# Optimization experiments

Measured on AMD Instinct MI355X. Metric: run time of the kernel, lower is better.

## Reference

```python
import jax, jax.numpy as jnp
import numpy as np

B, F, M, N, H, O = 8, 128, 256, 1024, 64, 128
BN_EPS = 1e-5
COS_EPS = 1e-8


def _bn(x, g, b, m, v):
    # inference-mode BatchNorm over channel axis 1
    shape = [1] * x.ndim
    shape[1] = -1
    return g.reshape(shape) * (x - m.reshape(shape)) * jax.lax.rsqrt(v.reshape(shape) + BN_EPS) + b.reshape(shape)


def setup_inputs() -> dict:
    key = jax.random.key(0)
    ks = jax.random.split(key, 24)
    def n(k, shape, s=1.0):
        return jax.random.normal(k, shape, dtype=jnp.float32) * s
    inp = {}
    inp['template_feature'] = n(ks[0], (B, F, M))
    inp['search_feature'] = n(ks[1], (B, F, N))
    # SharedMLP 1x1 conv weights (bias=False because bn=True)
    inp['W1'] = n(ks[2], (H, F + 1), 0.05)
    inp['W2'] = n(ks[3], (H, H), 0.05)
    inp['W3'] = n(ks[4], (H, H), 0.05)
    # fea_layer: conv1d(H, bn=True) then conv1d(O, activation=None, bias=True)
    inp['Wc1'] = n(ks[5], (H, H), 0.05)
    inp['Wc2'] = n(ks[6], (O, H), 0.05)
    inp['bc2'] = n(ks[7], (O,), 0.05)
    for i, nm in enumerate(['1', '2', '3', 'c1']):
        inp['g' + nm] = 1.0 + n(ks[8 + i], (H,), 0.1)
        inp['b' + nm] = n(ks[12 + i], (H,), 0.1)
        inp['m' + nm] = n(ks[16 + i], (H,), 0.01)
        inp['v' + nm] = jax.random.uniform(ks[20 + i], (H,), minval=0.5, maxval=1.5, dtype=jnp.float32)
    return inp


def reference(template_feature, search_feature, W1, W2, W3, Wc1, Wc2, bc2,
              g1, b1, m1, v1, g2, b2, m2, v2, g3, b3, m3, v3, gc1, bc1, mc1, vc1):
    t, s = template_feature, search_feature
    # pairwise cosine similarity over channel dim (no BxFxMxN expand needed)
    dot = jnp.einsum('bfm,bfn->bmn', t, s)
    nt = jnp.linalg.norm(t, axis=1)  # (B, M)
    ns = jnp.linalg.norm(s, axis=1)  # (B, N)
    cos = dot / jnp.maximum(nt[:, :, None] * ns[:, None, :], COS_EPS)  # (B, M, N)
    # first 1x1 conv on concat(cos, expand(t)) computed fused (no concat materialization)
    h = jnp.einsum('hf,bfm->bhm', W1[:, 1:], t)[..., None] + W1[:, 0][None, :, None, None] * cos[:, None]
    h = jax.nn.relu(_bn(h, g1, b1, m1, v1))  # (B, H, M, N)
    h = jax.nn.relu(_bn(jnp.einsum('gh,bhmn->bgmn', W2, h), g2, b2, m2, v2))
    h = jax.nn.relu(_bn(jnp.einsum('gh,bhmn->bgmn', W3, h), g3, b3, m3, v3))
    p = jnp.max(h, axis=2)  # max-pool over M -> (B, H, N)
    c = jax.nn.relu(_bn(jnp.einsum('gh,bhn->bgn', Wc1, p), gc1, bc1, mc1, vc1))
    return jnp.einsum('oh,bhn->bon', Wc2, c) + bc2[None, :, None]  # (B, O, N)
```

## Files before the change

### kernel.cpp

```cpp
#include <hip/hip_runtime.h>


#define BB 8
#define FF 128
#define MM 256
#define NN 1024
#define HH 64
#define OO 128
#define BN_EPS 1e-5f
#define COS_EPS 1e-8f

#define WS_U     0
#define WS_C2    64
#define WS_C3    128
#define WS_CC1   192
#define WS_W2H   256
#define WS_W3H   2304
#define WS_WC1F  8448
#define WS_A1    12544
#define WS_NT    143616
#define WS_NS    145664
#define WS_COSH  153856
#define WS_P     1202432
#define PS       524288

typedef _Float16 half2v __attribute__((ext_vector_type(2)));
typedef _Float16 half8  __attribute__((ext_vector_type(8)));
typedef __attribute__((ext_vector_type(4))) float f32x4;

__device__ __forceinline__ unsigned int pkh2(float a, float b){
  auto h = __builtin_amdgcn_cvt_pkrtz(a, b);
  return __builtin_bit_cast(unsigned int, h);
}
__device__ __forceinline__ half2v u2h(unsigned int u){
  return __builtin_bit_cast(half2v, u);
}
__device__ __forceinline__ unsigned int h2u(half2v v){
  return __builtin_bit_cast(unsigned int, v);
}
__device__ __forceinline__ unsigned int relu2(unsigned int d){
  half2v v = __builtin_elementwise_max(u2h(d), (half2v){(_Float16)0, (_Float16)0});
  return h2u(v);
}
__device__ __forceinline__ unsigned int bh1(unsigned int up, half2v c, unsigned int ap){
  half2v v = __builtin_elementwise_fma(u2h(up), c, u2h(ap));
  v = __builtin_elementwise_max(v, (half2v){(_Float16)0, (_Float16)0});
  return h2u(v);
}
__device__ __forceinline__ float dot4(float4 a, float4 b, float acc){
  acc = fmaf(a.x, b.x, acc); acc = fmaf(a.y, b.y, acc);
  acc = fmaf(a.z, b.z, acc); acc = fmaf(a.w, b.w, acc);
  return acc;
}

__global__ __launch_bounds__(256) void k_prep(const float* t_, const float* s_,
    const float* W1, const float* W2, const float* W3, const float* Wc1,
    const float* g1, const float* b1, const float* m1, const float* v1,
    const float* g2, const float* b2, const float* m2, const float* v2,
    const float* g3, const float* b3, const float* m3, const float* v3,
    const float* gc1,const float* bc1,const float* mc1,const float* vc1,
    float* ws){
  __shared__ float W1s[64][133];
  int t = threadIdx.x;
  int bx = blockIdx.x;
  if (bx < 256){
    int b = bx >> 5, m0 = (bx & 31)*8;
    for (int idx = t; idx < 8192; idx += 256){
      int h = idx >> 7, f = idx & 127;
      W1s[h][f] = W1[h*129 + 1 + f];
    }
    __syncthreads();
    int h = t & 63, mg = t >> 6;
    const float* tp = t_ + (size_t)b*FF*MM + m0 + mg*2;
    float acc0 = 0.f, acc1 = 0.f;
    for (int f = 0; f < FF; f++){
      float wv = W1s[h][f];
      float2 tv = *(const float2*)&tp[(size_t)f*MM];
      acc0 = fmaf(wv, tv.x, acc0); acc1 = fmaf(wv, tv.y, acc1);
    }
    float a1 = g1[h] / sqrtf(v1[h] + BN_EPS);
    float c1 = b1[h] - a1*m1[h];
    unsigned short* dst = (unsigned short*)(ws + WS_A1) + ((size_t)(b*MM + m0 + mg*2))*64 + h;
    dst[0]  = (unsigned short)(pkh2(fmaf(a1, acc0, c1), 0.f) & 0xFFFFu);
    dst[64] = (unsigned short)(pkh2(fmaf(a1, acc1, c1), 0.f) & 0xFFFFu);
  } else if (bx < 416){
    __shared__ float red[4][64];
    int x = t & 63, fq = t >> 6;
    int idx = (bx - 256)*64 + x;
    const float* ptr; size_t stride;
    if (idx < BB*MM){
      int b = idx >> 8, m = idx & 255;
      ptr = t_ + (size_t)b*FF*MM + m; stride = MM;
    } else {
      int j = idx - BB*MM;
      int b = j >> 10, n = j & 1023;
      ptr = s_ + (size_t)b*FF*NN + n; stride = NN;
    }
    float acc = 0.f;
    for (int f = fq*32; f < fq*32 + 32; f++){
      float v = ptr[(size_t)f*stride]; acc = fmaf(v, v, acc);
    }
    red[fq][x] = acc;
    __syncthreads();
    if (fq == 0)
      ws[WS_NT + idx] = sqrtf(red[0][x] + red[1][x] + red[2][x] + red[3][x]);
  } else {
    if (t < 64){
      float a1 = g1[t] / sqrtf(v1[t] + BN_EPS);
      ws[WS_U + t]   = a1 * W1[t*129];
      float a2 = g2[t] / sqrtf(v2[t] + BN_EPS);
      ws[WS_C2 + t]  = b2[t] - a2*m2[t];
      float a3 = g3[t] / sqrtf(v3[t] + BN_EPS);
      ws[WS_C3 + t]  = b3[t] - a3*m3[t];
      float ac = gc1[t] / sqrtf(vc1[t] + BN_EPS);
      ws[WS_CC1 + t] = bc1[t] - ac*mc1[t];
    }
    unsigned short* w2h = (unsigned short*)(ws + WS_W2H);
    unsigned short* w3h = (unsigned short*)(ws + WS_W3H);
    for (int i = t; i < 4096; i += 256){
      int g = i >> 6;
      float a2 = g2[g] / sqrtf(v2[g] + BN_EPS);
      w2h[i] = __builtin_bit_cast(unsigned short, (_Float16)(a2 * W2[i]));
      float a3 = g3[g] / sqrtf(v3[g] + BN_EPS);
      w3h[i] = __builtin_bit_cast(unsigned short, (_Float16)(a3 * W3[i]));
      float ac = gc1[g] / sqrtf(vc1[g] + BN_EPS);
      ws[WS_WC1F + i] = ac * Wc1[i];
    }
  }
}

__global__ __launch_bounds__(256) void k_cos(const float* t_, const float* s_, float* ws){
  __shared__ __align__(16) unsigned short tS[64][136];
  __shared__ __align__(16) unsigned short sS[64][136];
  __shared__ float ntS[64], nsS[64];
  int t = threadIdx.x;
  int lane = t & 63, w = t >> 6;
  int ln15 = lane & 15, quad = lane >> 4;
  int m0 = blockIdx.x*64, n0 = blockIdx.y*64, b = blockIdx.z;
  {
    int x = t & 63;
    const float* tb = t_ + (size_t)b*FF*MM + m0 + x;
    const float* sb = s_ + (size_t)b*FF*NN + n0 + x;
    #pragma unroll
    for (int k = 0; k < 16; k++){
      int fp = w*16 + k;
      *(unsigned int*)&tS[x][2*fp] = pkh2(tb[(size_t)(2*fp)*MM], tb[(size_t)(2*fp+1)*MM]);
      *(unsigned int*)&sS[x][2*fp] = pkh2(sb[(size_t)(2*fp)*NN], sb[(size_t)(2*fp+1)*NN]);
    }
    if (t < 64) ntS[t] = ws[WS_NT + b*MM + m0 + t];
    else if (t < 128) nsS[t-64] = ws[WS_NS + b*NN + n0 + (t-64)];
  }
  __syncthreads();
  half8 A4[4];
  #pragma unroll
  for (int kc = 0; kc < 4; kc++)
    A4[kc] = *(const half8*)&sS[w*16 + ln15][kc*32 + quad*8];
  float4 ns4 = *(const float4*)&nsS[w*16 + quad*4];
  int nb = n0 + w*16 + quad*4;
  unsigned short* cosw = (unsigned short*)(ws + WS_COSH);
  #pragma unroll
  for (int mt = 0; mt < 4; mt++){
    f32x4 acc = (f32x4){0.f,0.f,0.f,0.f};
    #pragma unroll
    for (int kc = 0; kc < 4; kc++){
      half8 B4 = *(const half8*)&tS[mt*16 + ln15][kc*32 + quad*8];
      acc = __builtin_amdgcn_mfma_f32_16x16x32_f16(A4[kc], B4, acc, 0, 0, 0);
    }
    int m = m0 + mt*16 + ln15;
    float ntv = ntS[mt*16 + ln15];
    float c0 = acc[0] * __builtin_amdgcn_rcpf(fmaxf(ntv*ns4.x, COS_EPS));
    float c1 = acc[1] * __builtin_amdgcn_rcpf(fmaxf(ntv*ns4.y, COS_EPS));
    float c2 = acc[2] * __builtin_amdgcn_rcpf(fmaxf(ntv*ns4.z, COS_EPS));
    float c3 = acc[3] * __builtin_amdgcn_rcpf(fmaxf(ntv*ns4.w, COS_EPS));
    uint2 vv;
    vv.x = pkh2(c0, c1);
    vv.y = pkh2(c2, c3);
    *(uint2*)&cosw[(size_t)(b*MM + m)*NN + nb] = vv;
  }
}

__global__ __launch_bounds__(256, 3) void k_main(const float* ws, float* Pp){
  __shared__ __align__(16) unsigned char h2B[4][2][2304];
  __shared__ __align__(16) float redS[3][16][68];
  int t = threadIdx.x;
  int lane = t & 63, w = t >> 6;
  int ln15 = lane & 15, quad = lane >> 4;
  int b = blockIdx.y;
  int n0 = blockIdx.x * 16;
  int ms = blockIdx.z;

  const unsigned short* w2h = (const unsigned short*)(ws + WS_W2H);
  const unsigned short* w3h = (const unsigned short*)(ws + WS_W3H);
  half8 W2A[4][2], W3A[4][2];
  f32x4 c2v[4];
  #pragma unroll
  for (int rt = 0; rt < 4; rt++){
    int g = rt*16 + ln15;
    #pragma unroll
    for (int kk = 0; kk < 2; kk++){
      W2A[rt][kk] = *(const half8*)&w2h[g*64 + kk*32 + quad*8];
      W3A[rt][kk] = *(const half8*)&w3h[g*64 + kk*32 + quad*8];
    }
    float4 cb2 = *(const float4*)&ws[WS_C2 + rt*16 + quad*4];
    c2v[rt] = (f32x4){cb2.x, cb2.y, cb2.z, cb2.w};
  }
  f32x4 zf = (f32x4){0.f, 0.f, 0.f, 0.f};
  unsigned int upk[2][4];
  #pragma unroll
  for (int kk = 0; kk < 2; kk++){
    float4 ua = *(const float4*)&ws[WS_U + kk*32 + quad*8];
    float4 ub = *(const float4*)&ws[WS_U + kk*32 + quad*8 + 4];
    upk[kk][0] = pkh2(ua.x, ua.y); upk[kk][1] = pkh2(ua.z, ua.w);
    upk[kk][2] = pkh2(ub.x, ub.y); upk[kk][3] = pkh2(ub.z, ub.w);
  }
  const unsigned short* A1H = (const unsigned short*)(ws + WS_A1) + (size_t)b*MM*64;
  int n = n0 + ln15;
  const unsigned short* cosP = (const unsigned short*)(ws + WS_COSH)
                               + (size_t)b*MM*NN + n;
  unsigned char* myb = &h2B[w][0][0];
  int wOff = ln15*144 + quad*8;
  int rOff = ln15*144 + quad*16;

  f32x4 p[4];
  #pragma unroll
  for (int rt = 0; rt < 4; rt++)
    p[rt] = (f32x4){-3.0e38f, -3.0e38f, -3.0e38f, -3.0e38f};

  int m0i = ms*128 + w;
  unsigned int cu = cosP[(size_t)m0i*NN];
  uint4 a1a = *(const uint4*)&A1H[(size_t)m0i*64 + quad*8];
  uint4 a1b = *(const uint4*)&A1H[(size_t)m0i*64 + 32 + quad*8];

  {
    int mN = ms*128 + 4 + w;
    unsigned int cuN = cosP[(size_t)mN*NN];
    uint4 a1aN = *(const uint4*)&A1H[(size_t)mN*64 + quad*8];
    uint4 a1bN = *(const uint4*)&A1H[(size_t)mN*64 + 32 + quad*8];
    unsigned int cd = cu | (cu << 16);
    half2v ch = u2h(cd);
    uint4 q0, q1;
    q0.x = bh1(upk[0][0], ch, a1a.x); q0.y = bh1(upk[0][1], ch, a1a.y);
    q0.z = bh1(upk[0][2], ch, a1a.z); q0.w = bh1(upk[0][3], ch, a1a.w);
    q1.x = bh1(upk[1][0], ch, a1b.x); q1.y = bh1(upk[1][1], ch, a1b.y);
    q1.z = bh1(upk[1][2], ch, a1b.z); q1.w = bh1(upk[1][3], ch, a1b.w);
    half8 b0h = __builtin_bit_cast(half8, q0);
    half8 b1h = __builtin_bit_cast(half8, q1);
    f32x4 acc[4];
    #pragma unroll
    for (int rt = 0; rt < 4; rt++){
      acc[rt] = __builtin_amdgcn_mfma_f32_16x16x32_f16(W2A[rt][0], b0h, c2v[rt], 0, 0, 0);
      acc[rt] = __builtin_amdgcn_mfma_f32_16x16x32_f16(W2A[rt][1], b1h, acc[rt], 0, 0, 0);
    }
    #pragma unroll
    for (int rt = 0; rt < 4; rt++){
      uint2 vv;
      vv.x = relu2(pkh2(acc[rt][0], acc[rt][1]));
      vv.y = relu2(pkh2(acc[rt][2], acc[rt][3]));
      *(uint2*)(myb + rt*32 + wOff) = vv;
    }
    cu = cuN; a1a = a1aN; a1b = a1bN;
  }

  for (int mc = 1; mc < 32; mc++){
    unsigned char* rb = myb + ((mc - 1) & 1)*2304;
    half8 pe0 = *(const half8*)(rb + rOff);
    half8 pe1 = *(const half8*)(rb + rOff + 64);

    int mN = ms*128 + (mc < 31 ? mc + 1 : 31)*4 + w;
    unsigned int cuN = cosP[(size_t)mN*NN];
    uint4 a1aN = *(const uint4*)&A1H[(size_t)mN*64 + quad*8];
    uint4 a1bN = *(const uint4*)&A1H[(size_t)mN*64 + 32 + quad*8];

    unsigned int cd = cu | (cu << 16);
    half2v ch = u2h(cd);
    uint4 q0, q1;
    q0.x = bh1(upk[0][0], ch, a1a.x); q0.y = bh1(upk[0][1], ch, a1a.y);
    q0.z = bh1(upk[0][2], ch, a1a.z); q0.w = bh1(upk[0][3], ch, a1a.w);
    q1.x = bh1(upk[1][0], ch, a1b.x); q1.y = bh1(upk[1][1], ch, a1b.y);
    q1.z = bh1(upk[1][2], ch, a1b.z); q1.w = bh1(upk[1][3], ch, a1b.w);
    half8 b0h = __builtin_bit_cast(half8, q0);
    half8 b1h = __builtin_bit_cast(half8, q1);

    f32x4 acc[4];
    #pragma unroll
    for (int rt = 0; rt < 4; rt++){
      acc[rt] = __builtin_amdgcn_mfma_f32_16x16x32_f16(W2A[rt][0], b0h, c2v[rt], 0, 0, 0);
      acc[rt] = __builtin_amdgcn_mfma_f32_16x16x32_f16(W2A[rt][1], b1h, acc[rt], 0, 0, 0);
    }

    #pragma unroll
    for (int rt = 0; rt < 4; rt++){
      f32x4 a3 = __builtin_amdgcn_mfma_f32_16x16x32_f16(W3A[rt][0], pe0, zf, 0, 0, 0);
      a3 = __builtin_amdgcn_mfma_f32_16x16x32_f16(W3A[rt][1], pe1, a3, 0, 0, 0);
      #pragma unroll
      for (int r = 0; r < 4; r++) p[rt][r] = fmaxf(p[rt][r], a3[r]);
    }

    unsigned char* wb = myb + (mc & 1)*2304;
    #pragma unroll
    for (int rt = 0; rt < 4; rt++){
      uint2 vv;
      vv.x = relu2(pkh2(acc[rt][0], acc[rt][1]));
      vv.y = relu2(pkh2(acc[rt][2], acc[rt][3]));
      *(uint2*)(wb + rt*32 + wOff) = vv;
    }
    cu = cuN; a1a = a1aN; a1b = a1bN;
  }

  {
    unsigned char* rb = myb + 2304;
    half8 pe0 = *(const half8*)(rb + rOff);
    half8 pe1 = *(const half8*)(rb + rOff + 64);
    #pragma unroll
    for (int rt = 0; rt < 4; rt++){
      f32x4 a3 = __builtin_amdgcn_mfma_f32_16x16x32_f16(W3A[rt][0], pe0, zf, 0, 0, 0);
      a3 = __builtin_amdgcn_mfma_f32_16x16x32_f16(W3A[rt][1], pe1, a3, 0, 0, 0);
      #pragma unroll
      for (int r = 0; r < 4; r++) p[rt][r] = fmaxf(p[rt][r], a3[r]);
    }
  }

  __syncthreads();
  if (w >= 1){
    #pragma unroll
    for (int rt = 0; rt < 4; rt++){
      f32x4 v = p[rt];
      *(float4*)&redS[w-1][ln15][rt*16 + quad*4] = make_float4(v[0], v[1], v[2], v[3]);
    }
  }
  __syncthreads();
  if (w == 0){
    float* Pb = Pp + (size_t)ms*PS + ((size_t)(b*NN + n) << 6);
    #pragma unroll
    for (int rt = 0; rt < 4; rt++){
      float4 o1 = *(const float4*)&redS[0][ln15][rt*16 + quad*4];
      float4 o2 = *(const float4*)&redS[1][ln15][rt*16 + quad*4];
      float4 o3 = *(const float4*)&redS[2][ln15][rt*16 + quad*4];
      float4 c3b = *(const float4*)&ws[WS_C3 + rt*16 + quad*4];
      float4 r4;
      r4.x = fmaxf(fmaxf(fmaxf(p[rt][0], o1.x), fmaxf(o2.x, o3.x)) + c3b.x, 0.f);
      r4.y = fmaxf(fmaxf(fmaxf(p[rt][1], o1.y), fmaxf(o2.y, o3.y)) + c3b.y, 0.f);
      r4.z = fmaxf(fmaxf(fmaxf(p[rt][2], o1.z), fmaxf(o2.z, o3.z)) + c3b.z, 0.f);
      r4.w = fmaxf(fmaxf(fmaxf(p[rt][3], o1.w), fmaxf(o2.w, o3.w)) + c3b.w, 0.f);
      *(float4*)&Pb[rt*16 + quad*4] = r4;
    }
  }
}

__global__ __launch_bounds__(256) void k_tail(const float* Wc2, const float* bc2,
                                              const float* ws, float* out){
  __shared__ float WT[64][68];
  __shared__ float pT[32][68];
  __shared__ float cS[32][68];
  int t = threadIdx.x;
  int n0 = blockIdx.x * 32;
  int b = blockIdx.y;
  for (int i = t; i < 4096; i += 256) WT[i >> 6][i & 63] = ws[WS_WC1F + i];
  const float* P0 = ws + WS_P + ((size_t)(b*NN + n0) << 6);
  const float* P1 = P0 + PS;
  for (int i = t; i < 2048; i += 256) pT[i >> 6][i & 63] = fmaxf(P0[i], P1[i]);
  __syncthreads();
  {
    int n = t & 31, q = t >> 5;
    for (int k = 0; k < 8; k++){
      int g = q*8 + k;
      float acc = ws[WS_CC1 + g];
      for (int hs = 0; hs < 64; hs += 4){
        float4 wv = *(const float4*)&WT[g][hs];
        float4 pv = *(const float4*)&pT[n][hs];
        acc = dot4(wv, pv, acc);
      }
      cS[n][g] = fmaxf(acc, 0.f);
    }
  }
  __syncthreads();
  {
    int o = t & 127, hf = t >> 7;
    float bco = bc2[o];
    float accO[16];
    #pragma unroll
    for (int i = 0; i < 16; i++) accO[i] = bco;
    for (int hs = 0; hs < 64; hs += 4){
      float4 w4 = *(const float4*)&Wc2[o*64 + hs];
      #pragma unroll
      for (int i = 0; i < 16; i++){
        float4 cv = *(const float4*)&cS[hf*16 + i][hs];
        accO[i] = dot4(w4, cv, accO[i]);
      }
    }
    #pragma unroll
    for (int i = 0; i < 16; i++)
      out[((size_t)(b*OO + o))*NN + n0 + hf*16 + i] = accO[i];
  }
}

extern "C" void kernel_launch(void* const* d_in, const int* in_sizes, int n_in,
                              void* d_out, int out_size, void* d_ws, size_t ws_size,
                              hipStream_t stream){
  (void)in_sizes; (void)n_in; (void)out_size; (void)ws_size;
  const float* t_  = (const float*)d_in[0];
  const float* s_  = (const float*)d_in[1];
  const float* W1  = (const float*)d_in[2];
  const float* W2  = (const float*)d_in[3];
  const float* W3  = (const float*)d_in[4];
  const float* Wc1 = (const float*)d_in[5];
  const float* Wc2 = (const float*)d_in[6];
  const float* bc2 = (const float*)d_in[7];
  const float* g1 = (const float*)d_in[8],  *b1 = (const float*)d_in[9],
             * m1 = (const float*)d_in[10], *v1 = (const float*)d_in[11];
  const float* g2 = (const float*)d_in[12], *b2 = (const float*)d_in[13],
             * m2 = (const float*)d_in[14], *v2 = (const float*)d_in[15];
  const float* g3 = (const float*)d_in[16], *b3 = (const float*)d_in[17],
             * m3 = (const float*)d_in[18], *v3 = (const float*)d_in[19];
  const float* gc1 = (const float*)d_in[20], *bc1 = (const float*)d_in[21],
             * mc1 = (const float*)d_in[22], *vc1 = (const float*)d_in[23];
  float* ws = (float*)d_ws;
  float* out = (float*)d_out;

  k_prep<<<417, 256, 0, stream>>>(t_, s_, W1, W2, W3, Wc1,
      g1,b1,m1,v1, g2,b2,m2,v2, g3,b3,m3,v3, gc1,bc1,mc1,vc1, ws);
  k_cos<<<dim3(4, 16, 8), 256, 0, stream>>>(t_, s_, ws);
  k_main<<<dim3(64, 8, 2), 256, 0, stream>>>(ws, ws + WS_P);
  k_tail<<<dim3(32, 8), 256, 0, stream>>>(Wc2, bc2, ws, out);
}
```

Baseline: 169.6 us.

## Feed layer-2 MFMA output directly into layer-3 MFMA via register layout

The layer-3 matmul now uses 16x16x16 MFMAs whose B-operand register layout matches the 16x16 accumulator layout of the layer-2 output, so the ReLU'd fp16 results are passed straight from registers. This removes the per-wave LDS staging buffer, the LDS write/read round trip and the double-buffered software pipeline with its prologue and epilogue. In exchange it issues twice as many (smaller) MFMAs for layer 3 and loses the one-iteration overlap between layer-2 and layer-3 work. Freeing LDS may also raise occupancy.

```diff
diff --git a/kernel.cpp b/kernel.cpp
--- a/kernel.cpp
+++ b/kernel.cpp
@@ -25,6 +25,7 @@
 #define PS       524288
 
 typedef _Float16 half2v __attribute__((ext_vector_type(2)));
+typedef _Float16 half4  __attribute__((ext_vector_type(4)));
 typedef _Float16 half8  __attribute__((ext_vector_type(8)));
 typedef __attribute__((ext_vector_type(4))) float f32x4;
 
@@ -180,7 +181,6 @@
 }
 
 __global__ __launch_bounds__(256, 3) void k_main(const float* ws, float* Pp){
-  __shared__ __align__(16) unsigned char h2B[4][2][2304];
   __shared__ __align__(16) float redS[3][16][68];
   int t = threadIdx.x;
   int lane = t & 63, w = t >> 6;
@@ -191,16 +191,18 @@
 
   const unsigned short* w2h = (const unsigned short*)(ws + WS_W2H);
   const unsigned short* w3h = (const unsigned short*)(ws + WS_W3H);
-  half8 W2A[4][2], W3A[4][2];
+  half8 W2A[4][2];
+  half4 W3A[4][4];
   f32x4 c2v[4];
   #pragma unroll
   for (int rt = 0; rt < 4; rt++){
     int g = rt*16 + ln15;
     #pragma unroll
-    for (int kk = 0; kk < 2; kk++){
+    for (int kk = 0; kk < 2; kk++)
       W2A[rt][kk] = *(const half8*)&w2h[g*64 + kk*32 + quad*8];
-      W3A[rt][kk] = *(const half8*)&w3h[g*64 + kk*32 + quad*8];
-    }
+    #pragma unroll
+    for (int ks = 0; ks < 4; ks++)
+      W3A[rt][ks] = *(const half4*)&w3h[g*64 + ks*16 + quad*4];
     float4 cb2 = *(const float4*)&ws[WS_C2 + rt*16 + quad*4];
     c2v[rt] = (f32x4){cb2.x, cb2.y, cb2.z, cb2.w};
   }
@@ -217,9 +219,6 @@
   int n = n0 + ln15;
   const unsigned short* cosP = (const unsigned short*)(ws + WS_COSH)
                                + (size_t)b*MM*NN + n;
-  unsigned char* myb = &h2B[w][0][0];
-  int wOff = ln15*144 + quad*8;
-  int rOff = ln15*144 + quad*16;
 
   f32x4 p[4];
   #pragma unroll
@@ -231,11 +230,12 @@
   uint4 a1a = *(const uint4*)&A1H[(size_t)m0i*64 + quad*8];
   uint4 a1b = *(const uint4*)&A1H[(size_t)m0i*64 + 32 + quad*8];
 
-  {
-    int mN = ms*128 + 4 + w;
+  for (int mc = 0; mc < 32; mc++){
+    int mN = ms*128 + (mc < 31 ? mc + 1 : 31)*4 + w;
     unsigned int cuN = cosP[(size_t)mN*NN];
     uint4 a1aN = *(const uint4*)&A1H[(size_t)mN*64 + quad*8];
     uint4 a1bN = *(const uint4*)&A1H[(size_t)mN*64 + 32 + quad*8];
+
     unsigned int cd = cu | (cu << 16);
     half2v ch = u2h(cd);
     uint4 q0, q1;
@@ -245,79 +245,34 @@
     q1.z = bh1(upk[1][2], ch, a1b.z); q1.w = bh1(upk[1][3], ch, a1b.w);
     half8 b0h = __builtin_bit_cast(half8, q0);
     half8 b1h = __builtin_bit_cast(half8, q1);
+
     f32x4 acc[4];
     #pragma unroll
     for (int rt = 0; rt < 4; rt++){
       acc[rt] = __builtin_amdgcn_mfma_f32_16x16x32_f16(W2A[rt][0], b0h, c2v[rt], 0, 0, 0);
       acc[rt] = __builtin_amdgcn_mfma_f32_16x16x32_f16(W2A[rt][1], b1h, acc[rt], 0, 0, 0);
     }
+
+    half4 pk[4];
+    #pragma unroll
+    for (int ks = 0; ks < 4; ks++){
+      uint2 vv;
+      vv.x = relu2(pkh2(acc[ks][0], acc[ks][1]));
+      vv.y = relu2(pkh2(acc[ks][2], acc[ks][3]));
+      pk[ks] = __builtin_bit_cast(half4, vv);
+    }
+
     #pragma unroll
     for (int rt = 0; rt < 4; rt++){
-      uint2 vv;
-      vv.x = relu2(pkh2(acc[rt][0], acc[rt][1]));
-      vv.y = relu2(pkh2(acc[rt][2], acc[rt][3]));
-      *(uint2*)(myb + rt*32 + wOff) = vv;
-    }
-    cu = cuN; a1a = a1aN; a1b = a1bN;
-  }
-
-  for (int mc = 1; mc < 32; mc++){
-    unsigned char* rb = myb + ((mc - 1) & 1)*2304;
-    half8 pe0 = *(const half8*)(rb + rOff);
-    half8 pe1 = *(const half8*)(rb + rOff + 64);
-
-    int mN = ms*128 + (mc < 31 ? mc + 1 : 31)*4 + w;
-    unsigned int cuN = cosP[(size_t)mN*NN];
-    uint4 a1aN = *(const uint4*)&A1H[(size_t)mN*64 + quad*8];
-    uint4 a1bN = *(const uint4*)&A1H[(size_t)mN*64 + 32 + quad*8];
-
-    unsigned int cd = cu | (cu << 16);
-    half2v ch = u2h(cd);
-    uint4 q0, q1;
-    q0.x = bh1(upk[0][0], ch, a1a.x); q0.y = bh1(upk[0][1], ch, a1a.y);
-    q0.z = bh1(upk[0][2], ch, a1a.z); q0.w = bh1(upk[0][3], ch, a1a.w);
-    q1.x = bh1(upk[1][0], ch, a1b.x); q1.y = bh1(upk[1][1], ch, a1b.y);
-    q1.z = bh1(upk[1][2], ch, a1b.z); q1.w = bh1(upk[1][3], ch, a1b.w);
-    half8 b0h = __builtin_bit_cast(half8, q0);
-    half8 b1h = __builtin_bit_cast(half8, q1);
-
-    f32x4 acc[4];
-    #pragma unroll
-    for (int rt = 0; rt < 4; rt++){
-      acc[rt] = __builtin_amdgcn_mfma_f32_16x16x32_f16(W2A[rt][0], b0h, c2v[rt], 0, 0, 0);
-      acc[rt] = __builtin_amdgcn_mfma_f32_16x16x32_f16(W2A[rt][1], b1h, acc[rt], 0, 0, 0);
-    }
-
-    #pragma unroll
-    for (int rt = 0; rt < 4; rt++){
-      f32x4 a3 = __builtin_amdgcn_mfma_f32_16x16x32_f16(W3A[rt][0], pe0, zf, 0, 0, 0);
-      a3 = __builtin_amdgcn_mfma_f32_16x16x32_f16(W3A[rt][1], pe1, a3, 0, 0, 0);
+      f32x4 a3 = __builtin_amdgcn_mfma_f32_16x16x16f16(W3A[rt][0], pk[0], zf, 0, 0, 0);
+      a3 = __builtin_amdgcn_mfma_f32_16x16x16f16(W3A[rt][1], pk[1], a3, 0, 0, 0);
+      a3 = __builtin_amdgcn_mfma_f32_16x16x16f16(W3A[rt][2], pk[2], a3, 0, 0, 0);
+      a3 = __builtin_amdgcn_mfma_f32_16x16x16f16(W3A[rt][3], pk[3], a3, 0, 0, 0);
       #pragma unroll
       for (int r = 0; r < 4; r++) p[rt][r] = fmaxf(p[rt][r], a3[r]);
     }
 
-    unsigned char* wb = myb + (mc & 1)*2304;
-    #pragma unroll
-    for (int rt = 0; rt < 4; rt++){
-      uint2 vv;
-      vv.x = relu2(pkh2(acc[rt][0], acc[rt][1]));
-      vv.y = relu2(pkh2(acc[rt][2], acc[rt][3]));
-      *(uint2*)(wb + rt*32 + wOff) = vv;
-    }
     cu = cuN; a1a = a1aN; a1b = a1bN;
-  }
-
-  {
-    unsigned char* rb = myb + 2304;
-    half8 pe0 = *(const half8*)(rb + rOff);
-    half8 pe1 = *(const half8*)(rb + rOff + 64);
-    #pragma unroll
-    for (int rt = 0; rt < 4; rt++){
-      f32x4 a3 = __builtin_amdgcn_mfma_f32_16x16x32_f16(W3A[rt][0], pe0, zf, 0, 0, 0);
-      a3 = __builtin_amdgcn_mfma_f32_16x16x32_f16(W3A[rt][1], pe1, a3, 0, 0, 0);
-      #pragma unroll
-      for (int r = 0; r < 4; r++) p[rt][r] = fmaxf(p[rt][r], a3[r]);
-    }
   }
 
   __syncthreads();
```

New measurement: 178.4 us. 1.05x slower.

## Keep layer-2 MFMA output in registers by permuting W3 columns

Applied to the files above, without the earlier changes.

The W3 half-precision weights are now stored with a permuted K ordering that matches the MFMA accumulator layout. The layer-2 outputs can then feed the layer-3 MFMA B operand straight from registers, with no round-trip through a per-wave LDS double buffer. This removes the LDS writes and reads and about 18KB of shared memory per block. It also moves the layer-3 MFMAs ahead of the layer-2 ones in each iteration, which could change register pressure and occupancy.

```diff
diff --git a/kernel.cpp b/kernel.cpp
--- a/kernel.cpp
+++ b/kernel.cpp
@@ -118,12 +118,17 @@
     unsigned short* w2h = (unsigned short*)(ws + WS_W2H);
     unsigned short* w3h = (unsigned short*)(ws + WS_W3H);
     for (int i = t; i < 4096; i += 256){
-      int g = i >> 6;
-      float a2 = g2[g] / sqrtf(v2[g] + BN_EPS);
+      int gp = i >> 6;
+      float a2 = g2[gp] / sqrtf(v2[gp] + BN_EPS);
       w2h[i] = __builtin_bit_cast(unsigned short, (_Float16)(a2 * W2[i]));
-      float a3 = g3[g] / sqrtf(v3[g] + BN_EPS);
-      w3h[i] = __builtin_bit_cast(unsigned short, (_Float16)(a3 * W3[i]));
-      float ac = gc1[g] / sqrtf(vc1[g] + BN_EPS);
+      {
+        int s = i & 63;
+        int kk = s >> 5, s2 = s & 31, q = s2 >> 3, j = s2 & 7;
+        int g = kk*32 + ((j < 4) ? (q*4 + j) : (16 + q*4 + (j - 4)));
+        float a3 = g3[gp] / sqrtf(v3[gp] + BN_EPS);
+        w3h[i] = __builtin_bit_cast(unsigned short, (_Float16)(a3 * W3[gp*64 + g]));
+      }
+      float ac = gc1[gp] / sqrtf(vc1[gp] + BN_EPS);
       ws[WS_WC1F + i] = ac * Wc1[i];
     }
   }
@@ -180,7 +185,6 @@
 }
 
 __global__ __launch_bounds__(256, 3) void k_main(const float* ws, float* Pp){
-  __shared__ __align__(16) unsigned char h2B[4][2][2304];
   __shared__ __align__(16) float redS[3][16][68];
   int t = threadIdx.x;
   int lane = t & 63, w = t >> 6;
@@ -217,9 +221,6 @@
   int n = n0 + ln15;
   const unsigned short* cosP = (const unsigned short*)(ws + WS_COSH)
                                + (size_t)b*MM*NN + n;
-  unsigned char* myb = &h2B[w][0][0];
-  int wOff = ln15*144 + quad*8;
-  int rOff = ln15*144 + quad*16;
 
   f32x4 p[4];
   #pragma unroll
@@ -230,6 +231,8 @@
   unsigned int cu = cosP[(size_t)m0i*NN];
   uint4 a1a = *(const uint4*)&A1H[(size_t)m0i*64 + quad*8];
   uint4 a1b = *(const uint4*)&A1H[(size_t)m0i*64 + 32 + quad*8];
+
+  uint4 e0P, e1P;
 
   {
     int mN = ms*128 + 4 + w;
@@ -251,25 +254,28 @@
       acc[rt] = __builtin_amdgcn_mfma_f32_16x16x32_f16(W2A[rt][0], b0h, c2v[rt], 0, 0, 0);
       acc[rt] = __builtin_amdgcn_mfma_f32_16x16x32_f16(W2A[rt][1], b1h, acc[rt], 0, 0, 0);
     }
-    #pragma unroll
-    for (int rt = 0; rt < 4; rt++){
-      uint2 vv;
-      vv.x = relu2(pkh2(acc[rt][0], acc[rt][1]));
-      vv.y = relu2(pkh2(acc[rt][2], acc[rt][3]));
-      *(uint2*)(myb + rt*32 + wOff) = vv;
-    }
+    e0P.x = relu2(pkh2(acc[0][0], acc[0][1])); e0P.y = relu2(pkh2(acc[0][2], acc[0][3]));
+    e0P.z = relu2(pkh2(acc[1][0], acc[1][1])); e0P.w = relu2(pkh2(acc[1][2], acc[1][3]));
+    e1P.x = relu2(pkh2(acc[2][0], acc[2][1])); e1P.y = relu2(pkh2(acc[2][2], acc[2][3]));
+    e1P.z = relu2(pkh2(acc[3][0], acc[3][1])); e1P.w = relu2(pkh2(acc[3][2], acc[3][3]));
     cu = cuN; a1a = a1aN; a1b = a1bN;
   }
 
   for (int mc = 1; mc < 32; mc++){
-    unsigned char* rb = myb + ((mc - 1) & 1)*2304;
-    half8 pe0 = *(const half8*)(rb + rOff);
-    half8 pe1 = *(const half8*)(rb + rOff + 64);
-
     int mN = ms*128 + (mc < 31 ? mc + 1 : 31)*4 + w;
     unsigned int cuN = cosP[(size_t)mN*NN];
     uint4 a1aN = *(const uint4*)&A1H[(size_t)mN*64 + quad*8];
     uint4 a1bN = *(const uint4*)&A1H[(size_t)mN*64 + 32 + quad*8];
+
+    half8 pe0 = __builtin_bit_cast(half8, e0P);
+    half8 pe1 = __builtin_bit_cast(half8, e1P);
+    #pragma unroll
+    for (int rt = 0; rt < 4; rt++){
+      f32x4 a3 = __builtin_amdgcn_mfma_f32_16x16x32_f16(W3A[rt][0], pe0, zf, 0, 0, 0);
+      a3 = __builtin_amdgcn_mfma_f32_16x16x32_f16(W3A[rt][1], pe1, a3, 0, 0, 0);
+      #pragma unroll
+      for (int r = 0; r < 4; r++) p[rt][r] = fmaxf(p[rt][r], a3[r]);
+    }
 
     unsigned int cd = cu | (cu << 16);
     half2v ch = u2h(cd);
@@ -288,29 +294,17 @@
       acc[rt] = __builtin_amdgcn_mfma_f32_16x16x32_f16(W2A[rt][1], b1h, acc[rt], 0, 0, 0);
     }
 
-    #pragma unroll
-    for (int rt = 0; rt < 4; rt++){
-      f32x4 a3 = __builtin_amdgcn_mfma_f32_16x16x32_f16(W3A[rt][0], pe0, zf, 0, 0, 0);
-      a3 = __builtin_amdgcn_mfma_f32_16x16x32_f16(W3A[rt][1], pe1, a3, 0, 0, 0);
-      #pragma unroll
-      for (int r = 0; r < 4; r++) p[rt][r] = fmaxf(p[rt][r], a3[r]);
-    }
-
-    unsigned char* wb = myb + (mc & 1)*2304;
-    #pragma unroll
-    for (int rt = 0; rt < 4; rt++){
-      uint2 vv;
-      vv.x = relu2(pkh2(acc[rt][0], acc[rt][1]));
-      vv.y = relu2(pkh2(acc[rt][2], acc[rt][3]));
-      *(uint2*)(wb + rt*32 + wOff) = vv;
-    }
+    e0P.x = relu2(pkh2(acc[0][0], acc[0][1])); e0P.y = relu2(pkh2(acc[0][2], acc[0][3]));
+    e0P.z = relu2(pkh2(acc[1][0], acc[1][1])); e0P.w = relu2(pkh2(acc[1][2], acc[1][3]));
+    e1P.x = relu2(pkh2(acc[2][0], acc[2][1])); e1P.y = relu2(pkh2(acc[2][2], acc[2][3]));
+    e1P.z = relu2(pkh2(acc[3][0], acc[3][1])); e1P.w = relu2(pkh2(acc[3][2], acc[3][3]));
+
     cu = cuN; a1a = a1aN; a1b = a1bN;
   }
 
   {
-    unsigned char* rb = myb + 2304;
-    half8 pe0 = *(const half8*)(rb + rOff);
-    half8 pe1 = *(const half8*)(rb + rOff + 64);
+    half8 pe0 = __builtin_bit_cast(half8, e0P);
+    half8 pe1 = __builtin_bit_cast(half8, e1P);
     #pragma unroll
     for (int rt = 0; rt < 4; rt++){
       f32x4 a3 = __builtin_amdgcn_mfma_f32_16x16x32_f16(W3A[rt][0], pe0, zf, 0, 0, 0);
```

New measurement: 169.2 us. Within noise of the previous version (-0.3%).
